# Performance work log

Measured on AMD Instinct MI355X. Metric: run time of the kernel, lower is better.

Reference implementation:

```python
import jax, jax.numpy as jnp
import numpy as np

N, F, H, L, O, E = 20000, 128, 128, 4, 64, 640000
NEG_SLOPE = 0.2  # PyG GATConv default


def setup_inputs() -> dict:
    key = jax.random.key(0)
    ks = jax.random.split(key, 8)
    x = jax.random.normal(ks[0], (N, F), dtype=jnp.float32)
    edge_index = jax.random.randint(ks[1], (2, E), 0, N, dtype=jnp.int64)
    sc = 1.0 / np.sqrt(F)
    Ws = jax.random.normal(ks[2], (L, F, H), dtype=jnp.float32) * sc
    att_src = jax.random.normal(ks[3], (L, H), dtype=jnp.float32) * sc
    att_dst = jax.random.normal(ks[4], (L, H), dtype=jnp.float32) * sc
    biases = jnp.zeros((L, H), dtype=jnp.float32)
    W_out = jax.random.normal(ks[5], (H, O), dtype=jnp.float32) * (1.0 / np.sqrt(H))
    b_out = jnp.zeros((O,), dtype=jnp.float32)
    return {"x": x, "edge_index": edge_index, "Ws": Ws, "att_src": att_src,
            "att_dst": att_dst, "biases": biases, "W_out": W_out, "b_out": b_out}


def _gat_conv(h, src, dst, W, a_s, a_d, b):
    # h: [N, F_in]; single-head GATConv (PyG semantics)
    z = h @ W                                   # [N, H]
    alpha_s = z @ a_s                           # [N]
    alpha_d = z @ a_d                           # [N]
    logits = jax.nn.leaky_relu(alpha_s[src] + alpha_d[dst], negative_slope=NEG_SLOPE)  # [E']
    # segment-softmax over edges grouped by destination node
    m = jax.ops.segment_max(logits, dst, num_segments=N)
    p = jnp.exp(logits - m[dst])
    s = jax.ops.segment_sum(p, dst, num_segments=N)
    alpha = p / (s[dst] + 1e-16)                # [E']
    out = jax.ops.segment_sum(alpha[:, None] * z[src], dst, num_segments=N)  # [N, H]
    return out + b


def reference(x, edge_index, Ws, att_src, att_dst, biases, W_out, b_out):
    # add self-loops once (PyG GATConv default add_self_loops=True)
    loop = jnp.arange(N, dtype=edge_index.dtype)
    src = jnp.concatenate([edge_index[0], loop])
    dst = jnp.concatenate([edge_index[1], loop])
    h = x
    for l in range(L):
        h = _gat_conv(h, src, dst, Ws[l], att_src[l], att_dst[l], biases[l])
        h = jax.nn.relu(h)  # Dropout is identity at eval
    return h @ W_out + b_out  # [N, O]
```

## Files before the change

### kernel.cpp

```cpp
#include <hip/hip_runtime.h>

#define NN 20000
#define FF 128
#define HH 128
#define LL 4
#define OO 64
#define EE 640000
#define NEG 0.2f
#define NB ((NN + 255) / 256)

typedef short bf16x8 __attribute__((ext_vector_type(8)));
typedef float f32x4 __attribute__((ext_vector_type(4)));

__device__ inline ushort f2bf(float f) {
    uint u = __float_as_uint(f);
    return (ushort)((u + 0x7fffu + ((u >> 16) & 1u)) >> 16);
}


__global__ void k_init_counters(int* __restrict__ counters) {
    int i = blockIdx.x * 256 + threadIdx.x;
    if (i < NN) counters[i] = 1;
}

__global__ void k_hist(const int* __restrict__ dst, int* __restrict__ counters) {
    int e = blockIdx.x * 256 + threadIdx.x;
    if (e < EE) atomicAdd(&counters[dst[e]], 1);
}

__global__ void k_partial(const int* __restrict__ counters, int* __restrict__ partials) {
    __shared__ int ws[4];
    int t = threadIdx.x;
    int i = blockIdx.x * 256 + t;
    int c = (i < NN) ? counters[i] : 0;
    #pragma unroll
    for (int off = 32; off; off >>= 1) c += __shfl_xor(c, off);
    if ((t & 63) == 0) ws[t >> 6] = c;
    __syncthreads();
    if (t == 0) partials[blockIdx.x] = ws[0] + ws[1] + ws[2] + ws[3];
}

__global__ void k_scan_small(const int* __restrict__ partials, int* __restrict__ offsets) {
    __shared__ int sp[128];
    int t = threadIdx.x;
    int v = (t < NB) ? partials[t] : 0;
    sp[t] = v;
    __syncthreads();
    for (int off = 1; off < 128; off <<= 1) {
        int u = (t >= off) ? sp[t - off] : 0;
        __syncthreads();
        sp[t] += u;
        __syncthreads();
    }
    if (t < NB) offsets[t] = sp[t] - v;
}

__global__ void k_apply(const int* __restrict__ counters, const int* __restrict__ offsets,
                        int* __restrict__ row_off, int* __restrict__ cursor,
                        int* __restrict__ src_sorted) {
    __shared__ int sc[256];
    int t = threadIdx.x;
    int i = blockIdx.x * 256 + t;
    int c = (i < NN) ? counters[i] : 0;
    sc[t] = c;
    __syncthreads();
    for (int off = 1; off < 256; off <<= 1) {
        int u = (t >= off) ? sc[t - off] : 0;
        __syncthreads();
        sc[t] += u;
        __syncthreads();
    }
    int incl = sc[t];
    int base = offsets[blockIdx.x];
    if (i < NN) {
        int excl = base + incl - c;
        row_off[i] = excl;
        cursor[i] = excl + 1;
        src_sorted[excl] = i;
        if (i == NN - 1) row_off[NN] = base + incl;
    }
}

__global__ void k_scatter(const int* __restrict__ src, const int* __restrict__ dst,
                          int* __restrict__ cursor, int* __restrict__ src_sorted) {
    int e = blockIdx.x * 256 + threadIdx.x;
    if (e < EE) {
        int p = atomicAdd(&cursor[dst[e]], 1);
        src_sorted[p] = src[e];
    }
}


__global__ void k_convw(const float* __restrict__ Ws, const float* __restrict__ Wout,
                        ushort* __restrict__ wh, ushort* __restrict__ wl) {
    int idx = blockIdx.x * 256 + threadIdx.x;
    const int per_l = HH * 128;
    float v;
    if (idx < LL * per_l) {
        int l = idx / per_l, rem = idx % per_l;
        int n = rem >> 7, k = rem & 127;
        v = Ws[(size_t)l * 128 * HH + (size_t)k * HH + n];
    } else {
        int j = idx - LL * per_l;
        if (j >= OO * 128) return;
        int n = j >> 7, k = j & 127;
        v = Wout[(size_t)k * OO + n];
    }
    ushort h = f2bf(v);
    float hf = __uint_as_float((uint)h << 16);
    wh[idx] = h;
    wl[idx] = f2bf(v - hf);
}


__global__ void k_wa(const float* __restrict__ Ws, const float* __restrict__ attS,
                     const float* __restrict__ attD, float* __restrict__ wa) {
    int t = blockIdx.x * 256 + threadIdx.x;
    if (t >= LL * 256) return;
    int l = t >> 8, rem = t & 255, which = rem >> 7, k = rem & 127;
    const float* wrow = Ws + (size_t)l * 128 * HH + (size_t)k * HH;
    const float* av = (which ? attD : attS) + l * HH;
    float s = 0.f;
    #pragma unroll 4
    for (int n = 0; n < HH; n++) s += wrow[n] * av[n];
    wa[l * 256 + which * 128 + k] = s;
}


template <int NCOL, bool BIAS, bool ALPHAS>
__global__ void k_gemm_mfma(const float* __restrict__ A, const ushort* __restrict__ wh,
                            const ushort* __restrict__ wl, const float* __restrict__ bias,
                            float* __restrict__ C, const float* __restrict__ wa,
                            float* __restrict__ as_out, float* __restrict__ ad_out) {
    constexpr int CT = NCOL / 32;
    int bid = blockIdx.x;
    int rt = bid / CT, ct = bid % CT;
    int l = threadIdx.x;
    int row0 = rt * 16, col0 = ct * 32;
    int lr = l & 15, lg = l >> 4;

    const float* arow = A + (size_t)(row0 + lr) * 128;
    f32x4 af0[4], af1[4];
    #pragma unroll
    for (int s = 0; s < 4; s++) {
        af0[s] = *(const f32x4*)(arow + s * 32 + lg * 8);
        af1[s] = *(const f32x4*)(arow + s * 32 + lg * 8 + 4);
    }
    bf16x8 ah[4], al[4];
    #pragma unroll
    for (int s = 0; s < 4; s++) {
        #pragma unroll
        for (int j = 0; j < 8; j++) {
            float v = (j < 4) ? af0[s][j] : af1[s][j - 4];
            ushort h = f2bf(v);
            float hf = __uint_as_float((uint)h << 16);
            ah[s][j] = (short)h;
            al[s][j] = (short)f2bf(v - hf);
        }
    }

    f32x4 acc[2] = {{0.f, 0.f, 0.f, 0.f}, {0.f, 0.f, 0.f, 0.f}};

    #pragma unroll
    for (int s = 0; s < 4; s++) {
        #pragma unroll
        for (int nt = 0; nt < 2; nt++) {
            int woff = (col0 + nt * 16 + lr) * 128 + s * 32 + lg * 8;
            bf16x8 bh = *(const bf16x8*)(wh + woff);
            bf16x8 bl = *(const bf16x8*)(wl + woff);
            acc[nt] = __builtin_amdgcn_mfma_f32_16x16x32_bf16(ah[s], bh, acc[nt], 0, 0, 0);
            acc[nt] = __builtin_amdgcn_mfma_f32_16x16x32_bf16(ah[s], bl, acc[nt], 0, 0, 0);
            acc[nt] = __builtin_amdgcn_mfma_f32_16x16x32_bf16(al[s], bh, acc[nt], 0, 0, 0);
        }
    }

    int orow = lg * 4;
    #pragma unroll
    for (int nt = 0; nt < 2; nt++) {
        #pragma unroll
        for (int r = 0; r < 4; r++) {
            float v = acc[nt][r];
            if (BIAS) v += bias[col0 + nt * 16 + lr];
            C[(size_t)(row0 + orow + r) * NCOL + col0 + nt * 16 + lr] = v;
        }
    }

    if constexpr (ALPHAS) {
        if (ct == 0) {
            float ps = 0.f, pd = 0.f;
            #pragma unroll
            for (int s = 0; s < 4; s++) {
                #pragma unroll
                for (int j = 0; j < 8; j++) {
                    float v = (j < 4) ? af0[s][j] : af1[s][j - 4];
                    int k = s * 32 + lg * 8 + j;
                    ps += v * wa[k];
                    pd += v * wa[128 + k];
                }
            }
            ps += __shfl_xor(ps, 16);  pd += __shfl_xor(pd, 16);
            ps += __shfl_xor(ps, 32);  pd += __shfl_xor(pd, 32);
            if (lg == 0) {
                as_out[row0 + lr] = ps;
                ad_out[row0 + lr] = pd;
            }
        }
    }
}


__global__ void k_aggregate(const float* __restrict__ z, const float* __restrict__ as,
                            const float* __restrict__ ad, const int* __restrict__ row_off,
                            const int* __restrict__ srcs, const float* __restrict__ bias,
                            float* __restrict__ out) {
    int node = blockIdx.x * 4 + (threadIdx.x >> 6);
    int lane = threadIdx.x & 63;
    if (node >= NN) return;
    int beg = row_off[node], end = row_off[node + 1];
    float adn = ad[node];
    float lself = as[node] + adn;
    float mx = (lself >= 0.f) ? lself : NEG * lself;

    int g = lane >> 5, cl = lane & 31;
    const float4* zb = (const float4*)z;
    float4 acc = make_float4(0.f, 0.f, 0.f, 0.f);
    float s = 0.f;

    for (int e = beg + g; e < end; e += 16) {
        int e1 = e + 2, e2 = e + 4, e3 = e + 6, e4 = e + 8, e5 = e + 10, e6 = e + 12, e7 = e + 14;
        int lim = end - 1;
        int i1 = min(e1, lim), i2 = min(e2, lim), i3 = min(e3, lim);
        int i4 = min(e4, lim), i5 = min(e5, lim), i6 = min(e6, lim), i7 = min(e7, lim);
        int s0 = srcs[e], s1 = srcs[i1], s2 = srcs[i2], s3 = srcs[i3];
        int s4 = srcs[i4], s5 = srcs[i5], s6 = srcs[i6], s7 = srcs[i7];
        float l0 = as[s0] + adn, l1 = as[s1] + adn, l2 = as[s2] + adn, l3 = as[s3] + adn;
        float l4 = as[s4] + adn, l5 = as[s5] + adn, l6 = as[s6] + adn, l7 = as[s7] + adn;
        l0 = (l0 >= 0.f) ? l0 : NEG * l0;  l1 = (l1 >= 0.f) ? l1 : NEG * l1;
        l2 = (l2 >= 0.f) ? l2 : NEG * l2;  l3 = (l3 >= 0.f) ? l3 : NEG * l3;
        l4 = (l4 >= 0.f) ? l4 : NEG * l4;  l5 = (l5 >= 0.f) ? l5 : NEG * l5;
        l6 = (l6 >= 0.f) ? l6 : NEG * l6;  l7 = (l7 >= 0.f) ? l7 : NEG * l7;
        float4 z0 = zb[(size_t)s0 * 32 + cl];
        float4 z1 = zb[(size_t)s1 * 32 + cl];
        float4 z2 = zb[(size_t)s2 * 32 + cl];
        float4 z3 = zb[(size_t)s3 * 32 + cl];
        float4 z4 = zb[(size_t)s4 * 32 + cl];
        float4 z5 = zb[(size_t)s5 * 32 + cl];
        float4 z6 = zb[(size_t)s6 * 32 + cl];
        float4 z7 = zb[(size_t)s7 * 32 + cl];
        float p0 = __expf(l0 - mx);
        float p1 = (e1 < end) ? __expf(l1 - mx) : 0.f;
        float p2 = (e2 < end) ? __expf(l2 - mx) : 0.f;
        float p3 = (e3 < end) ? __expf(l3 - mx) : 0.f;
        float p4 = (e4 < end) ? __expf(l4 - mx) : 0.f;
        float p5 = (e5 < end) ? __expf(l5 - mx) : 0.f;
        float p6 = (e6 < end) ? __expf(l6 - mx) : 0.f;
        float p7 = (e7 < end) ? __expf(l7 - mx) : 0.f;
        s += ((p0 + p1) + (p2 + p3)) + ((p4 + p5) + (p6 + p7));
        acc.x += (p0 * z0.x + p1 * z1.x + p2 * z2.x + p3 * z3.x)
               + (p4 * z4.x + p5 * z5.x + p6 * z6.x + p7 * z7.x);
        acc.y += (p0 * z0.y + p1 * z1.y + p2 * z2.y + p3 * z3.y)
               + (p4 * z4.y + p5 * z5.y + p6 * z6.y + p7 * z7.y);
        acc.z += (p0 * z0.z + p1 * z1.z + p2 * z2.z + p3 * z3.z)
               + (p4 * z4.z + p5 * z5.z + p6 * z6.z + p7 * z7.z);
        acc.w += (p0 * z0.w + p1 * z1.w + p2 * z2.w + p3 * z3.w)
               + (p4 * z4.w + p5 * z5.w + p6 * z6.w + p7 * z7.w);
    }

    acc.x += __shfl_xor(acc.x, 32);
    acc.y += __shfl_xor(acc.y, 32);
    acc.z += __shfl_xor(acc.z, 32);
    acc.w += __shfl_xor(acc.w, 32);
    s     += __shfl_xor(s, 32);

    if (g == 0) {
        float inv = 1.f / (s + 1e-16f);
        float4 b = ((const float4*)bias)[cl];
        float4 o;
        o.x = fmaxf(acc.x * inv + b.x, 0.f);
        o.y = fmaxf(acc.y * inv + b.y, 0.f);
        o.z = fmaxf(acc.z * inv + b.z, 0.f);
        o.w = fmaxf(acc.w * inv + b.w, 0.f);
        ((float4*)out)[(size_t)node * 32 + cl] = o;
    }
}


extern "C" void kernel_launch(void* const* d_in, const int* in_sizes, int n_in,
                              void* d_out, int out_size, void* d_ws, size_t ws_size,
                              hipStream_t stream) {
    const float* x      = (const float*)d_in[0];
    const int*   ei     = (const int*)d_in[1];
    const float* Ws     = (const float*)d_in[2];
    const float* attS   = (const float*)d_in[3];
    const float* attD   = (const float*)d_in[4];
    const float* biases = (const float*)d_in[5];
    const float* W_out  = (const float*)d_in[6];
    const float* b_out  = (const float*)d_in[7];
    float* out = (float*)d_out;

    const int* srcp = ei;
    const int* dstp = ei + EE;

    char* w = (char*)d_ws;
    auto take = [&](size_t bytes) {
        char* p = w;
        w += (bytes + 15) & ~(size_t)15;
        return p;
    };
    float*  zbuf       = (float*)take((size_t)NN * HH * 4);
    float*  hbuf       = (float*)take((size_t)NN * HH * 4);
    float*  as_v       = (float*)take((size_t)NN * 4);
    float*  ad_v       = (float*)take((size_t)NN * 4);
    int*    counters   = (int*)take((size_t)NN * 4);
    int*    row_off    = (int*)take((size_t)(NN + 1) * 4);
    int*    cursor     = (int*)take((size_t)NN * 4);
    int*    src_sorted = (int*)take((size_t)(EE + NN) * 4);
    int*    partials   = (int*)take((size_t)NB * 4);
    int*    offsets    = (int*)take((size_t)NB * 4);
    const int WTOT = LL * HH * 128 + OO * 128;
    ushort* whbuf      = (ushort*)take((size_t)WTOT * 2);
    ushort* wlbuf      = (ushort*)take((size_t)WTOT * 2);
    float*  wabuf      = (float*)take((size_t)LL * 256 * 4);

    k_init_counters<<<(NN + 255) / 256, 256, 0, stream>>>(counters);
    k_hist<<<(EE + 255) / 256, 256, 0, stream>>>(dstp, counters);
    k_partial<<<NB, 256, 0, stream>>>(counters, partials);
    k_scan_small<<<1, 128, 0, stream>>>(partials, offsets);
    k_apply<<<NB, 256, 0, stream>>>(counters, offsets, row_off, cursor, src_sorted);
    k_scatter<<<(EE + 255) / 256, 256, 0, stream>>>(srcp, dstp, cursor, src_sorted);
    k_convw<<<(WTOT + 255) / 256, 256, 0, stream>>>(Ws, W_out, whbuf, wlbuf);
    k_wa<<<(LL * 256 + 255) / 256, 256, 0, stream>>>(Ws, attS, attD, wabuf);

    const int node_blocks = (NN + 3) / 4;

    for (int l = 0; l < LL; l++) {
        const float* hin = (l == 0) ? x : hbuf;
        k_gemm_mfma<HH, false, true><<<(NN / 16) * (HH / 32), 64, 0, stream>>>(
            hin, whbuf + (size_t)l * HH * 128, wlbuf + (size_t)l * HH * 128,
            nullptr, zbuf, wabuf + l * 256, as_v, ad_v);
        k_aggregate<<<node_blocks, 256, 0, stream>>>(zbuf, as_v, ad_v, row_off, src_sorted,
                                                     biases + l * HH, hbuf);
    }

    k_gemm_mfma<OO, true, false><<<(NN / 16) * (OO / 32), 64, 0, stream>>>(
        hbuf, whbuf + (size_t)LL * HH * 128, wlbuf + (size_t)LL * HH * 128,
        b_out, out, nullptr, nullptr, nullptr);
}
```

Baseline: 329.9 us.

## Fuse aggregation with next layer's GEMM via shared-memory tile

```diff
diff --git a/kernel.cpp b/kernel.cpp
--- a/kernel.cpp
+++ b/kernel.cpp
@@ -8,6 +8,7 @@
 #define EE 640000
 #define NEG 0.2f
 #define NB ((NN + 255) / 256)
+#define NTILES (NN / 16)
 
 typedef short bf16x8 __attribute__((ext_vector_type(8)));
 typedef float f32x4 __attribute__((ext_vector_type(4)));
@@ -127,24 +128,95 @@
 }
 
 
+__device__ inline void do_agg(const float* __restrict__ z, const float* __restrict__ as,
+                              const float* __restrict__ ad, const int* __restrict__ row_off,
+                              const int* __restrict__ srcs, const float* __restrict__ bias,
+                              float (*h)[132], int node0, int wid, int l64) {
+    int g = l64 >> 5, cl = l64 & 31;
+    const float4* zb = (const float4*)z;
+    #pragma unroll 1
+    for (int i = 0; i < 4; i++) {
+        int node = node0 + wid * 4 + i;
+        int beg = row_off[node], end = row_off[node + 1];
+        float adn = ad[node];
+        float lself = as[node] + adn;
+        float mx = (lself >= 0.f) ? lself : NEG * lself;
+
+        float4 acc = make_float4(0.f, 0.f, 0.f, 0.f);
+        float s = 0.f;
+        for (int e = beg + g; e < end; e += 16) {
+            int e1 = e + 2, e2 = e + 4, e3 = e + 6, e4 = e + 8, e5 = e + 10, e6 = e + 12, e7 = e + 14;
+            int lim = end - 1;
+            int i1 = min(e1, lim), i2 = min(e2, lim), i3 = min(e3, lim);
+            int i4 = min(e4, lim), i5 = min(e5, lim), i6 = min(e6, lim), i7 = min(e7, lim);
+            int s0 = srcs[e], s1 = srcs[i1], s2 = srcs[i2], s3 = srcs[i3];
+            int s4 = srcs[i4], s5 = srcs[i5], s6 = srcs[i6], s7 = srcs[i7];
+            float l0 = as[s0] + adn, l1 = as[s1] + adn, l2 = as[s2] + adn, l3 = as[s3] + adn;
+            float l4 = as[s4] + adn, l5 = as[s5] + adn, l6 = as[s6] + adn, l7 = as[s7] + adn;
+            l0 = (l0 >= 0.f) ? l0 : NEG * l0;  l1 = (l1 >= 0.f) ? l1 : NEG * l1;
+            l2 = (l2 >= 0.f) ? l2 : NEG * l2;  l3 = (l3 >= 0.f) ? l3 : NEG * l3;
+            l4 = (l4 >= 0.f) ? l4 : NEG * l4;  l5 = (l5 >= 0.f) ? l5 : NEG * l5;
+            l6 = (l6 >= 0.f) ? l6 : NEG * l6;  l7 = (l7 >= 0.f) ? l7 : NEG * l7;
+            float4 z0 = zb[(size_t)s0 * 32 + cl];
+            float4 z1 = zb[(size_t)s1 * 32 + cl];
+            float4 z2 = zb[(size_t)s2 * 32 + cl];
+            float4 z3 = zb[(size_t)s3 * 32 + cl];
+            float4 z4 = zb[(size_t)s4 * 32 + cl];
+            float4 z5 = zb[(size_t)s5 * 32 + cl];
+            float4 z6 = zb[(size_t)s6 * 32 + cl];
+            float4 z7 = zb[(size_t)s7 * 32 + cl];
+            float p0 = __expf(l0 - mx);
+            float p1 = (e1 < end) ? __expf(l1 - mx) : 0.f;
+            float p2 = (e2 < end) ? __expf(l2 - mx) : 0.f;
+            float p3 = (e3 < end) ? __expf(l3 - mx) : 0.f;
+            float p4 = (e4 < end) ? __expf(l4 - mx) : 0.f;
+            float p5 = (e5 < end) ? __expf(l5 - mx) : 0.f;
+            float p6 = (e6 < end) ? __expf(l6 - mx) : 0.f;
+            float p7 = (e7 < end) ? __expf(l7 - mx) : 0.f;
+            s += ((p0 + p1) + (p2 + p3)) + ((p4 + p5) + (p6 + p7));
+            acc.x += (p0 * z0.x + p1 * z1.x + p2 * z2.x + p3 * z3.x)
+                   + (p4 * z4.x + p5 * z5.x + p6 * z6.x + p7 * z7.x);
+            acc.y += (p0 * z0.y + p1 * z1.y + p2 * z2.y + p3 * z3.y)
+                   + (p4 * z4.y + p5 * z5.y + p6 * z6.y + p7 * z7.y);
+            acc.z += (p0 * z0.z + p1 * z1.z + p2 * z2.z + p3 * z3.z)
+                   + (p4 * z4.z + p5 * z5.z + p6 * z6.z + p7 * z7.z);
+            acc.w += (p0 * z0.w + p1 * z1.w + p2 * z2.w + p3 * z3.w)
+                   + (p4 * z4.w + p5 * z5.w + p6 * z6.w + p7 * z7.w);
+        }
+        acc.x += __shfl_xor(acc.x, 32);
+        acc.y += __shfl_xor(acc.y, 32);
+        acc.z += __shfl_xor(acc.z, 32);
+        acc.w += __shfl_xor(acc.w, 32);
+        s     += __shfl_xor(s, 32);
+        if (g == 0) {
+            float inv = 1.f / (s + 1e-16f);
+            float4 b = ((const float4*)bias)[cl];
+            int lrow = wid * 4 + i;
+            h[lrow][cl * 4 + 0] = fmaxf(acc.x * inv + b.x, 0.f);
+            h[lrow][cl * 4 + 1] = fmaxf(acc.y * inv + b.y, 0.f);
+            h[lrow][cl * 4 + 2] = fmaxf(acc.z * inv + b.z, 0.f);
+            h[lrow][cl * 4 + 3] = fmaxf(acc.w * inv + b.w, 0.f);
+        }
+    }
+}
+
 template <int NCOL, bool BIAS, bool ALPHAS>
-__global__ void k_gemm_mfma(const float* __restrict__ A, const ushort* __restrict__ wh,
-                            const ushort* __restrict__ wl, const float* __restrict__ bias,
-                            float* __restrict__ C, const float* __restrict__ wa,
-                            float* __restrict__ as_out, float* __restrict__ ad_out) {
+__device__ inline void do_gemm(const float (*h)[132], const ushort* __restrict__ wh,
+                               const ushort* __restrict__ wl, const float* __restrict__ bias,
+                               float* __restrict__ C, const float* __restrict__ wa,
+                               float* __restrict__ as_o, float* __restrict__ ad_o,
+                               int row0, int wid, int l64) {
     constexpr int CT = NCOL / 32;
-    int bid = blockIdx.x;
-    int rt = bid / CT, ct = bid % CT;
-    int l = threadIdx.x;
-    int row0 = rt * 16, col0 = ct * 32;
-    int lr = l & 15, lg = l >> 4;
-
-    const float* arow = A + (size_t)(row0 + lr) * 128;
+    if (CT < 4 && wid >= CT) return;
+    int ct = wid;
+    int lr = l64 & 15, lg = l64 >> 4;
+    int col0 = ct * 32;
+
     f32x4 af0[4], af1[4];
     #pragma unroll
     for (int s = 0; s < 4; s++) {
-        af0[s] = *(const f32x4*)(arow + s * 32 + lg * 8);
-        af1[s] = *(const f32x4*)(arow + s * 32 + lg * 8 + 4);
+        af0[s] = *(const f32x4*)&h[lr][s * 32 + lg * 8];
+        af1[s] = *(const f32x4*)&h[lr][s * 32 + lg * 8 + 4];
     }
     bf16x8 ah[4], al[4];
     #pragma unroll
@@ -152,15 +224,14 @@
         #pragma unroll
         for (int j = 0; j < 8; j++) {
             float v = (j < 4) ? af0[s][j] : af1[s][j - 4];
-            ushort h = f2bf(v);
-            float hf = __uint_as_float((uint)h << 16);
-            ah[s][j] = (short)h;
+            ushort hb = f2bf(v);
+            float hf = __uint_as_float((uint)hb << 16);
+            ah[s][j] = (short)hb;
             al[s][j] = (short)f2bf(v - hf);
         }
     }
 
     f32x4 acc[2] = {{0.f, 0.f, 0.f, 0.f}, {0.f, 0.f, 0.f, 0.f}};
-
     #pragma unroll
     for (int s = 0; s < 4; s++) {
         #pragma unroll
@@ -201,87 +272,43 @@
             ps += __shfl_xor(ps, 16);  pd += __shfl_xor(pd, 16);
             ps += __shfl_xor(ps, 32);  pd += __shfl_xor(pd, 32);
             if (lg == 0) {
-                as_out[row0 + lr] = ps;
-                ad_out[row0 + lr] = pd;
+                as_o[row0 + lr] = ps;
+                ad_o[row0 + lr] = pd;
             }
         }
     }
 }
 
 
-__global__ void k_aggregate(const float* __restrict__ z, const float* __restrict__ as,
-                            const float* __restrict__ ad, const int* __restrict__ row_off,
-                            const int* __restrict__ srcs, const float* __restrict__ bias,
-                            float* __restrict__ out) {
-    int node = blockIdx.x * 4 + (threadIdx.x >> 6);
-    int lane = threadIdx.x & 63;
-    if (node >= NN) return;
-    int beg = row_off[node], end = row_off[node + 1];
-    float adn = ad[node];
-    float lself = as[node] + adn;
-    float mx = (lself >= 0.f) ? lself : NEG * lself;
-
-    int g = lane >> 5, cl = lane & 31;
-    const float4* zb = (const float4*)z;
-    float4 acc = make_float4(0.f, 0.f, 0.f, 0.f);
-    float s = 0.f;
-
-    for (int e = beg + g; e < end; e += 16) {
-        int e1 = e + 2, e2 = e + 4, e3 = e + 6, e4 = e + 8, e5 = e + 10, e6 = e + 12, e7 = e + 14;
-        int lim = end - 1;
-        int i1 = min(e1, lim), i2 = min(e2, lim), i3 = min(e3, lim);
-        int i4 = min(e4, lim), i5 = min(e5, lim), i6 = min(e6, lim), i7 = min(e7, lim);
-        int s0 = srcs[e], s1 = srcs[i1], s2 = srcs[i2], s3 = srcs[i3];
-        int s4 = srcs[i4], s5 = srcs[i5], s6 = srcs[i6], s7 = srcs[i7];
-        float l0 = as[s0] + adn, l1 = as[s1] + adn, l2 = as[s2] + adn, l3 = as[s3] + adn;
-        float l4 = as[s4] + adn, l5 = as[s5] + adn, l6 = as[s6] + adn, l7 = as[s7] + adn;
-        l0 = (l0 >= 0.f) ? l0 : NEG * l0;  l1 = (l1 >= 0.f) ? l1 : NEG * l1;
-        l2 = (l2 >= 0.f) ? l2 : NEG * l2;  l3 = (l3 >= 0.f) ? l3 : NEG * l3;
-        l4 = (l4 >= 0.f) ? l4 : NEG * l4;  l5 = (l5 >= 0.f) ? l5 : NEG * l5;
-        l6 = (l6 >= 0.f) ? l6 : NEG * l6;  l7 = (l7 >= 0.f) ? l7 : NEG * l7;
-        float4 z0 = zb[(size_t)s0 * 32 + cl];
-        float4 z1 = zb[(size_t)s1 * 32 + cl];
-        float4 z2 = zb[(size_t)s2 * 32 + cl];
-        float4 z3 = zb[(size_t)s3 * 32 + cl];
-        float4 z4 = zb[(size_t)s4 * 32 + cl];
-        float4 z5 = zb[(size_t)s5 * 32 + cl];
-        float4 z6 = zb[(size_t)s6 * 32 + cl];
-        float4 z7 = zb[(size_t)s7 * 32 + cl];
-        float p0 = __expf(l0 - mx);
-        float p1 = (e1 < end) ? __expf(l1 - mx) : 0.f;
-        float p2 = (e2 < end) ? __expf(l2 - mx) : 0.f;
-        float p3 = (e3 < end) ? __expf(l3 - mx) : 0.f;
-        float p4 = (e4 < end) ? __expf(l4 - mx) : 0.f;
-        float p5 = (e5 < end) ? __expf(l5 - mx) : 0.f;
-        float p6 = (e6 < end) ? __expf(l6 - mx) : 0.f;
-        float p7 = (e7 < end) ? __expf(l7 - mx) : 0.f;
-        s += ((p0 + p1) + (p2 + p3)) + ((p4 + p5) + (p6 + p7));
-        acc.x += (p0 * z0.x + p1 * z1.x + p2 * z2.x + p3 * z3.x)
-               + (p4 * z4.x + p5 * z5.x + p6 * z6.x + p7 * z7.x);
-        acc.y += (p0 * z0.y + p1 * z1.y + p2 * z2.y + p3 * z3.y)
-               + (p4 * z4.y + p5 * z5.y + p6 * z6.y + p7 * z7.y);
-        acc.z += (p0 * z0.z + p1 * z1.z + p2 * z2.z + p3 * z3.z)
-               + (p4 * z4.z + p5 * z5.z + p6 * z6.z + p7 * z7.z);
-        acc.w += (p0 * z0.w + p1 * z1.w + p2 * z2.w + p3 * z3.w)
-               + (p4 * z4.w + p5 * z5.w + p6 * z6.w + p7 * z7.w);
-    }
-
-    acc.x += __shfl_xor(acc.x, 32);
-    acc.y += __shfl_xor(acc.y, 32);
-    acc.z += __shfl_xor(acc.z, 32);
-    acc.w += __shfl_xor(acc.w, 32);
-    s     += __shfl_xor(s, 32);
-
-    if (g == 0) {
-        float inv = 1.f / (s + 1e-16f);
-        float4 b = ((const float4*)bias)[cl];
-        float4 o;
-        o.x = fmaxf(acc.x * inv + b.x, 0.f);
-        o.y = fmaxf(acc.y * inv + b.y, 0.f);
-        o.z = fmaxf(acc.z * inv + b.z, 0.f);
-        o.w = fmaxf(acc.w * inv + b.w, 0.f);
-        ((float4*)out)[(size_t)node * 32 + cl] = o;
-    }
+__global__ __launch_bounds__(256)
+void k_layer0(const float* __restrict__ x, const ushort* __restrict__ wh,
+              const ushort* __restrict__ wl, const float* __restrict__ wa,
+              float* __restrict__ z, float* __restrict__ as_o, float* __restrict__ ad_o) {
+    __shared__ float h[16][132];
+    int t = threadIdx.x, wid = t >> 6, l64 = t & 63;
+    int row0 = blockIdx.x * 16;
+    for (int i = t; i < 16 * 32; i += 256) {
+        int r = i >> 5, c4 = (i & 31) << 2;
+        *(float4*)&h[r][c4] = *(const float4*)&x[(size_t)(row0 + r) * 128 + c4];
+    }
+    __syncthreads();
+    do_gemm<HH, false, true>(h, wh, wl, nullptr, z, wa, as_o, ad_o, row0, wid, l64);
+}
+
+template <int NCOL, bool BIAS, bool ALPHAS>
+__global__ __launch_bounds__(256)
+void k_layer(const float* __restrict__ zin, const float* __restrict__ asi,
+             const float* __restrict__ adi, const int* __restrict__ row_off,
+             const int* __restrict__ srcs, const float* __restrict__ abias,
+             const ushort* __restrict__ wh, const ushort* __restrict__ wl,
+             const float* __restrict__ cbias, const float* __restrict__ wa,
+             float* __restrict__ zout, float* __restrict__ as_o, float* __restrict__ ad_o) {
+    __shared__ float h[16][132];
+    int t = threadIdx.x, wid = t >> 6, l64 = t & 63;
+    int row0 = blockIdx.x * 16;
+    do_agg(zin, asi, adi, row_off, srcs, abias, h, row0, wid, l64);
+    __syncthreads();
+    do_gemm<NCOL, BIAS, ALPHAS>(h, wh, wl, cbias, zout, wa, as_o, ad_o, row0, wid, l64);
 }
 
 
@@ -307,10 +334,12 @@
         w += (bytes + 15) & ~(size_t)15;
         return p;
     };
-    float*  zbuf       = (float*)take((size_t)NN * HH * 4);
-    float*  hbuf       = (float*)take((size_t)NN * HH * 4);
-    float*  as_v       = (float*)take((size_t)NN * 4);
-    float*  ad_v       = (float*)take((size_t)NN * 4);
+    float*  za         = (float*)take((size_t)NN * HH * 4);
+    float*  zbv        = (float*)take((size_t)NN * HH * 4);
+    float*  asa        = (float*)take((size_t)NN * 4);
+    float*  ada        = (float*)take((size_t)NN * 4);
+    float*  asb        = (float*)take((size_t)NN * 4);
+    float*  adb        = (float*)take((size_t)NN * 4);
     int*    counters   = (int*)take((size_t)NN * 4);
     int*    row_off    = (int*)take((size_t)(NN + 1) * 4);
     int*    cursor     = (int*)take((size_t)NN * 4);
@@ -331,18 +360,23 @@
     k_convw<<<(WTOT + 255) / 256, 256, 0, stream>>>(Ws, W_out, whbuf, wlbuf);
     k_wa<<<(LL * 256 + 255) / 256, 256, 0, stream>>>(Ws, attS, attD, wabuf);
 
-    const int node_blocks = (NN + 3) / 4;
-
-    for (int l = 0; l < LL; l++) {
-        const float* hin = (l == 0) ? x : hbuf;
-        k_gemm_mfma<HH, false, true><<<(NN / 16) * (HH / 32), 64, 0, stream>>>(
-            hin, whbuf + (size_t)l * HH * 128, wlbuf + (size_t)l * HH * 128,
-            nullptr, zbuf, wabuf + l * 256, as_v, ad_v);
-        k_aggregate<<<node_blocks, 256, 0, stream>>>(zbuf, as_v, ad_v, row_off, src_sorted,
-                                                     biases + l * HH, hbuf);
-    }
-
-    k_gemm_mfma<OO, true, false><<<(NN / 16) * (OO / 32), 64, 0, stream>>>(
-        hbuf, whbuf + (size_t)LL * HH * 128, wlbuf + (size_t)LL * HH * 128,
-        b_out, out, nullptr, nullptr, nullptr);
-}
+    k_layer0<<<NTILES, 256, 0, stream>>>(x, whbuf, wlbuf, wabuf, za, asa, ada);
+
+    k_layer<HH, false, true><<<NTILES, 256, 0, stream>>>(
+        za, asa, ada, row_off, src_sorted, biases + 0 * HH,
+        whbuf + (size_t)1 * HH * 128, wlbuf + (size_t)1 * HH * 128,
+        nullptr, wabuf + 1 * 256, zbv, asb, adb);
+    k_layer<HH, false, true><<<NTILES, 256, 0, stream>>>(
+        zbv, asb, adb, row_off, src_sorted, biases + 1 * HH,
+        whbuf + (size_t)2 * HH * 128, wlbuf + (size_t)2 * HH * 128,
+        nullptr, wabuf + 2 * 256, za, asa, ada);
+    k_layer<HH, false, true><<<NTILES, 256, 0, stream>>>(
+        za, asa, ada, row_off, src_sorted, biases + 2 * HH,
+        whbuf + (size_t)3 * HH * 128, wlbuf + (size_t)3 * HH * 128,
+        nullptr, wabuf + 3 * 256, zbv, asb, adb);
+
+    k_layer<OO, true, false><<<NTILES, 256, 0, stream>>>(
+        zbv, asb, adb, row_off, src_sorted, biases + 3 * HH,
+        whbuf + (size_t)LL * HH * 128, wlbuf + (size_t)LL * HH * 128,
+        b_out, nullptr, out, nullptr, nullptr);
+}
```

Measured after the change: 377.2 us. 14.3% more time.

## Precompute edge softmax weights per layer and restructure GEMM to stage rows in LDS

Applied to the files above, without the earlier changes.

```diff
diff --git a/kernel.cpp b/kernel.cpp
--- a/kernel.cpp
+++ b/kernel.cpp
@@ -6,8 +6,10 @@
 #define LL 4
 #define OO 64
 #define EE 640000
+#define ET (EE + NN)
 #define NEG 0.2f
 #define NB ((NN + 255) / 256)
+#define NTILES (NN / 16)
 
 typedef short bf16x8 __attribute__((ext_vector_type(8)));
 typedef float f32x4 __attribute__((ext_vector_type(4)));
@@ -57,7 +59,7 @@
 
 __global__ void k_apply(const int* __restrict__ counters, const int* __restrict__ offsets,
                         int* __restrict__ row_off, int* __restrict__ cursor,
-                        int* __restrict__ src_sorted) {
+                        int* __restrict__ src_sorted, int* __restrict__ dst_sorted) {
     __shared__ int sc[256];
     int t = threadIdx.x;
     int i = blockIdx.x * 256 + t;
@@ -77,16 +79,20 @@
         row_off[i] = excl;
         cursor[i] = excl + 1;
         src_sorted[excl] = i;
+        dst_sorted[excl] = i;
         if (i == NN - 1) row_off[NN] = base + incl;
     }
 }
 
 __global__ void k_scatter(const int* __restrict__ src, const int* __restrict__ dst,
-                          int* __restrict__ cursor, int* __restrict__ src_sorted) {
+                          int* __restrict__ cursor, int* __restrict__ src_sorted,
+                          int* __restrict__ dst_sorted) {
     int e = blockIdx.x * 256 + threadIdx.x;
     if (e < EE) {
-        int p = atomicAdd(&cursor[dst[e]], 1);
-        src_sorted[p] = src[e];
+        int d = dst[e];
+        int pidx = atomicAdd(&cursor[d], 1);
+        src_sorted[pidx] = src[e];
+        dst_sorted[pidx] = d;
     }
 }
 
@@ -127,24 +133,109 @@
 }
 
 
+__global__ void k_ew(const float* __restrict__ asv, const float* __restrict__ adv,
+                     const int* __restrict__ srcs, const int* __restrict__ dsts,
+                     float* __restrict__ p) {
+    int e = blockIdx.x * 256 + threadIdx.x;
+    if (e >= ET) return;
+    int s = srcs[e], d = dsts[e];
+    float ad_ = adv[d];
+    float ls = asv[s] + ad_;  ls = (ls >= 0.f) ? ls : NEG * ls;
+    float ld = asv[d] + ad_;  ld = (ld >= 0.f) ? ld : NEG * ld;
+    p[e] = __expf(ls - ld);
+}
+
+
+__global__ __launch_bounds__(256)
+void k_agg(const float* __restrict__ z, const float* __restrict__ p,
+           const int* __restrict__ row_off, const int* __restrict__ srcs,
+           const float* __restrict__ bias, float* __restrict__ h) {
+    int node = blockIdx.x * 4 + (threadIdx.x >> 6);
+    int l64 = threadIdx.x & 63;
+    if (node >= NN) return;
+    int g = l64 >> 5, cl = l64 & 31;
+    int beg = row_off[node], end = row_off[node + 1], lim = end - 1;
+    const float4* zb = (const float4*)z;
+
+    float4 acc = make_float4(0.f, 0.f, 0.f, 0.f);
+    float s = 0.f;
+    for (int e = beg + g * 8; e < end; e += 16) {
+        int i1 = min(e + 1, lim), i2 = min(e + 2, lim), i3 = min(e + 3, lim);
+        int i4 = min(e + 4, lim), i5 = min(e + 5, lim), i6 = min(e + 6, lim), i7 = min(e + 7, lim);
+        int s0 = srcs[e],  s1 = srcs[i1], s2 = srcs[i2], s3 = srcs[i3];
+        int s4 = srcs[i4], s5 = srcs[i5], s6 = srcs[i6], s7 = srcs[i7];
+        float p0 = p[e];
+        float p1 = (e + 1 < end) ? p[e + 1] : 0.f;
+        float p2 = (e + 2 < end) ? p[e + 2] : 0.f;
+        float p3 = (e + 3 < end) ? p[e + 3] : 0.f;
+        float p4 = (e + 4 < end) ? p[e + 4] : 0.f;
+        float p5 = (e + 5 < end) ? p[e + 5] : 0.f;
+        float p6 = (e + 6 < end) ? p[e + 6] : 0.f;
+        float p7 = (e + 7 < end) ? p[e + 7] : 0.f;
+        float4 z0 = zb[(size_t)s0 * 32 + cl];
+        float4 z1 = zb[(size_t)s1 * 32 + cl];
+        float4 z2 = zb[(size_t)s2 * 32 + cl];
+        float4 z3 = zb[(size_t)s3 * 32 + cl];
+        float4 z4 = zb[(size_t)s4 * 32 + cl];
+        float4 z5 = zb[(size_t)s5 * 32 + cl];
+        float4 z6 = zb[(size_t)s6 * 32 + cl];
+        float4 z7 = zb[(size_t)s7 * 32 + cl];
+        s += ((p0 + p1) + (p2 + p3)) + ((p4 + p5) + (p6 + p7));
+        acc.x += (p0 * z0.x + p1 * z1.x + p2 * z2.x + p3 * z3.x)
+               + (p4 * z4.x + p5 * z5.x + p6 * z6.x + p7 * z7.x);
+        acc.y += (p0 * z0.y + p1 * z1.y + p2 * z2.y + p3 * z3.y)
+               + (p4 * z4.y + p5 * z5.y + p6 * z6.y + p7 * z7.y);
+        acc.z += (p0 * z0.z + p1 * z1.z + p2 * z2.z + p3 * z3.z)
+               + (p4 * z4.z + p5 * z5.z + p6 * z6.z + p7 * z7.z);
+        acc.w += (p0 * z0.w + p1 * z1.w + p2 * z2.w + p3 * z3.w)
+               + (p4 * z4.w + p5 * z5.w + p6 * z6.w + p7 * z7.w);
+    }
+
+    acc.x += __shfl_xor(acc.x, 32);
+    acc.y += __shfl_xor(acc.y, 32);
+    acc.z += __shfl_xor(acc.z, 32);
+    acc.w += __shfl_xor(acc.w, 32);
+    s     += __shfl_xor(s, 32);
+
+    if (g == 0) {
+        float inv = 1.f / (s + 1e-16f);
+        float4 b = ((const float4*)bias)[cl];
+        float4 o;
+        o.x = fmaxf(acc.x * inv + b.x, 0.f);
+        o.y = fmaxf(acc.y * inv + b.y, 0.f);
+        o.z = fmaxf(acc.z * inv + b.z, 0.f);
+        o.w = fmaxf(acc.w * inv + b.w, 0.f);
+        ((float4*)h)[(size_t)node * 32 + cl] = o;
+    }
+}
+
+
 template <int NCOL, bool BIAS, bool ALPHAS>
-__global__ void k_gemm_mfma(const float* __restrict__ A, const ushort* __restrict__ wh,
-                            const ushort* __restrict__ wl, const float* __restrict__ bias,
-                            float* __restrict__ C, const float* __restrict__ wa,
-                            float* __restrict__ as_out, float* __restrict__ ad_out) {
+__global__ __launch_bounds__(256)
+void k_gemm2(const float* __restrict__ A, const ushort* __restrict__ wh,
+             const ushort* __restrict__ wl, const float* __restrict__ bias,
+             float* __restrict__ C, const float* __restrict__ wa,
+             float* __restrict__ as_o, float* __restrict__ ad_o) {
+    __shared__ float h[16][132];
+    int t = threadIdx.x;
+    int row0 = blockIdx.x * 16;
+    for (int i = t; i < 512; i += 256) {
+        int r = i >> 5, c4 = (i & 31) << 2;
+        *(float4*)&h[r][c4] = *(const float4*)&A[(size_t)(row0 + r) * 128 + c4];
+    }
+    __syncthreads();
+
+    int wid = t >> 6, l64 = t & 63;
     constexpr int CT = NCOL / 32;
-    int bid = blockIdx.x;
-    int rt = bid / CT, ct = bid % CT;
-    int l = threadIdx.x;
-    int row0 = rt * 16, col0 = ct * 32;
-    int lr = l & 15, lg = l >> 4;
-
-    const float* arow = A + (size_t)(row0 + lr) * 128;
+    if (wid >= CT) return;
+    int lr = l64 & 15, lg = l64 >> 4;
+    int col0 = wid * 32;
+
     f32x4 af0[4], af1[4];
     #pragma unroll
     for (int s = 0; s < 4; s++) {
-        af0[s] = *(const f32x4*)(arow + s * 32 + lg * 8);
-        af1[s] = *(const f32x4*)(arow + s * 32 + lg * 8 + 4);
+        af0[s] = *(const f32x4*)&h[lr][s * 32 + lg * 8];
+        af1[s] = *(const f32x4*)&h[lr][s * 32 + lg * 8 + 4];
     }
     bf16x8 ah[4], al[4];
     #pragma unroll
@@ -152,15 +243,14 @@
         #pragma unroll
         for (int j = 0; j < 8; j++) {
             float v = (j < 4) ? af0[s][j] : af1[s][j - 4];
-            ushort h = f2bf(v);
-            float hf = __uint_as_float((uint)h << 16);
-            ah[s][j] = (short)h;
+            ushort hb = f2bf(v);
+            float hf = __uint_as_float((uint)hb << 16);
+            ah[s][j] = (short)hb;
             al[s][j] = (short)f2bf(v - hf);
         }
     }
 
     f32x4 acc[2] = {{0.f, 0.f, 0.f, 0.f}, {0.f, 0.f, 0.f, 0.f}};
-
     #pragma unroll
     for (int s = 0; s < 4; s++) {
         #pragma unroll
@@ -177,16 +267,17 @@
     int orow = lg * 4;
     #pragma unroll
     for (int nt = 0; nt < 2; nt++) {
+        int c = col0 + nt * 16 + lr;
         #pragma unroll
         for (int r = 0; r < 4; r++) {
             float v = acc[nt][r];
-            if (BIAS) v += bias[col0 + nt * 16 + lr];
-            C[(size_t)(row0 + orow + r) * NCOL + col0 + nt * 16 + lr] = v;
+            if (BIAS) v += bias[c];
+            C[(size_t)(row0 + orow + r) * NCOL + c] = v;
         }
     }
 
     if constexpr (ALPHAS) {
-        if (ct == 0) {
+        if (wid == 0) {
             float ps = 0.f, pd = 0.f;
             #pragma unroll
             for (int s = 0; s < 4; s++) {
@@ -201,86 +292,10 @@
             ps += __shfl_xor(ps, 16);  pd += __shfl_xor(pd, 16);
             ps += __shfl_xor(ps, 32);  pd += __shfl_xor(pd, 32);
             if (lg == 0) {
-                as_out[row0 + lr] = ps;
-                ad_out[row0 + lr] = pd;
+                as_o[row0 + lr] = ps;
+                ad_o[row0 + lr] = pd;
             }
         }
-    }
-}
-
-
-__global__ void k_aggregate(const float* __restrict__ z, const float* __restrict__ as,
-                            const float* __restrict__ ad, const int* __restrict__ row_off,
-                            const int* __restrict__ srcs, const float* __restrict__ bias,
-                            float* __restrict__ out) {
-    int node = blockIdx.x * 4 + (threadIdx.x >> 6);
-    int lane = threadIdx.x & 63;
-    if (node >= NN) return;
-    int beg = row_off[node], end = row_off[node + 1];
-    float adn = ad[node];
-    float lself = as[node] + adn;
-    float mx = (lself >= 0.f) ? lself : NEG * lself;
-
-    int g = lane >> 5, cl = lane & 31;
-    const float4* zb = (const float4*)z;
-    float4 acc = make_float4(0.f, 0.f, 0.f, 0.f);
-    float s = 0.f;
-
-    for (int e = beg + g; e < end; e += 16) {
-        int e1 = e + 2, e2 = e + 4, e3 = e + 6, e4 = e + 8, e5 = e + 10, e6 = e + 12, e7 = e + 14;
-        int lim = end - 1;
-        int i1 = min(e1, lim), i2 = min(e2, lim), i3 = min(e3, lim);
-        int i4 = min(e4, lim), i5 = min(e5, lim), i6 = min(e6, lim), i7 = min(e7, lim);
-        int s0 = srcs[e], s1 = srcs[i1], s2 = srcs[i2], s3 = srcs[i3];
-        int s4 = srcs[i4], s5 = srcs[i5], s6 = srcs[i6], s7 = srcs[i7];
-        float l0 = as[s0] + adn, l1 = as[s1] + adn, l2 = as[s2] + adn, l3 = as[s3] + adn;
-        float l4 = as[s4] + adn, l5 = as[s5] + adn, l6 = as[s6] + adn, l7 = as[s7] + adn;
-        l0 = (l0 >= 0.f) ? l0 : NEG * l0;  l1 = (l1 >= 0.f) ? l1 : NEG * l1;
-        l2 = (l2 >= 0.f) ? l2 : NEG * l2;  l3 = (l3 >= 0.f) ? l3 : NEG * l3;
-        l4 = (l4 >= 0.f) ? l4 : NEG * l4;  l5 = (l5 >= 0.f) ? l5 : NEG * l5;
-        l6 = (l6 >= 0.f) ? l6 : NEG * l6;  l7 = (l7 >= 0.f) ? l7 : NEG * l7;
-        float4 z0 = zb[(size_t)s0 * 32 + cl];
-        float4 z1 = zb[(size_t)s1 * 32 + cl];
-        float4 z2 = zb[(size_t)s2 * 32 + cl];
-        float4 z3 = zb[(size_t)s3 * 32 + cl];
-        float4 z4 = zb[(size_t)s4 * 32 + cl];
-        float4 z5 = zb[(size_t)s5 * 32 + cl];
-        float4 z6 = zb[(size_t)s6 * 32 + cl];
-        float4 z7 = zb[(size_t)s7 * 32 + cl];
-        float p0 = __expf(l0 - mx);
-        float p1 = (e1 < end) ? __expf(l1 - mx) : 0.f;
-        float p2 = (e2 < end) ? __expf(l2 - mx) : 0.f;
-        float p3 = (e3 < end) ? __expf(l3 - mx) : 0.f;
-        float p4 = (e4 < end) ? __expf(l4 - mx) : 0.f;
-        float p5 = (e5 < end) ? __expf(l5 - mx) : 0.f;
-        float p6 = (e6 < end) ? __expf(l6 - mx) : 0.f;
-        float p7 = (e7 < end) ? __expf(l7 - mx) : 0.f;
-        s += ((p0 + p1) + (p2 + p3)) + ((p4 + p5) + (p6 + p7));
-        acc.x += (p0 * z0.x + p1 * z1.x + p2 * z2.x + p3 * z3.x)
-               + (p4 * z4.x + p5 * z5.x + p6 * z6.x + p7 * z7.x);
-        acc.y += (p0 * z0.y + p1 * z1.y + p2 * z2.y + p3 * z3.y)
-               + (p4 * z4.y + p5 * z5.y + p6 * z6.y + p7 * z7.y);
-        acc.z += (p0 * z0.z + p1 * z1.z + p2 * z2.z + p3 * z3.z)
-               + (p4 * z4.z + p5 * z5.z + p6 * z6.z + p7 * z7.z);
-        acc.w += (p0 * z0.w + p1 * z1.w + p2 * z2.w + p3 * z3.w)
-               + (p4 * z4.w + p5 * z5.w + p6 * z6.w + p7 * z7.w);
-    }
-
-    acc.x += __shfl_xor(acc.x, 32);
-    acc.y += __shfl_xor(acc.y, 32);
-    acc.z += __shfl_xor(acc.z, 32);
-    acc.w += __shfl_xor(acc.w, 32);
-    s     += __shfl_xor(s, 32);
-
-    if (g == 0) {
-        float inv = 1.f / (s + 1e-16f);
-        float4 b = ((const float4*)bias)[cl];
-        float4 o;
-        o.x = fmaxf(acc.x * inv + b.x, 0.f);
-        o.y = fmaxf(acc.y * inv + b.y, 0.f);
-        o.z = fmaxf(acc.z * inv + b.z, 0.f);
-        o.w = fmaxf(acc.w * inv + b.w, 0.f);
-        ((float4*)out)[(size_t)node * 32 + cl] = o;
     }
 }
 
@@ -307,14 +322,19 @@
         w += (bytes + 15) & ~(size_t)15;
         return p;
     };
-    float*  zbuf       = (float*)take((size_t)NN * HH * 4);
+    float*  za         = (float*)take((size_t)NN * HH * 4);
+    float*  zbv        = (float*)take((size_t)NN * HH * 4);
     float*  hbuf       = (float*)take((size_t)NN * HH * 4);
-    float*  as_v       = (float*)take((size_t)NN * 4);
-    float*  ad_v       = (float*)take((size_t)NN * 4);
+    float*  asa        = (float*)take((size_t)NN * 4);
+    float*  ada        = (float*)take((size_t)NN * 4);
+    float*  asb        = (float*)take((size_t)NN * 4);
+    float*  adb        = (float*)take((size_t)NN * 4);
     int*    counters   = (int*)take((size_t)NN * 4);
     int*    row_off    = (int*)take((size_t)(NN + 1) * 4);
     int*    cursor     = (int*)take((size_t)NN * 4);
-    int*    src_sorted = (int*)take((size_t)(EE + NN) * 4);
+    int*    src_sorted = (int*)take((size_t)ET * 4);
+    int*    dst_sorted = (int*)take((size_t)ET * 4);
+    float*  pbuf       = (float*)take((size_t)ET * 4);
     int*    partials   = (int*)take((size_t)NB * 4);
     int*    offsets    = (int*)take((size_t)NB * 4);
     const int WTOT = LL * HH * 128 + OO * 128;
@@ -326,23 +346,38 @@
     k_hist<<<(EE + 255) / 256, 256, 0, stream>>>(dstp, counters);
     k_partial<<<NB, 256, 0, stream>>>(counters, partials);
     k_scan_small<<<1, 128, 0, stream>>>(partials, offsets);
-    k_apply<<<NB, 256, 0, stream>>>(counters, offsets, row_off, cursor, src_sorted);
-    k_scatter<<<(EE + 255) / 256, 256, 0, stream>>>(srcp, dstp, cursor, src_sorted);
+    k_apply<<<NB, 256, 0, stream>>>(counters, offsets, row_off, cursor,
+                                    src_sorted, dst_sorted);
+    k_scatter<<<(EE + 255) / 256, 256, 0, stream>>>(srcp, dstp, cursor,
+                                                    src_sorted, dst_sorted);
     k_convw<<<(WTOT + 255) / 256, 256, 0, stream>>>(Ws, W_out, whbuf, wlbuf);
     k_wa<<<(LL * 256 + 255) / 256, 256, 0, stream>>>(Ws, attS, attD, wabuf);
 
-    const int node_blocks = (NN + 3) / 4;
-
-    for (int l = 0; l < LL; l++) {
-        const float* hin = (l == 0) ? x : hbuf;
-        k_gemm_mfma<HH, false, true><<<(NN / 16) * (HH / 32), 64, 0, stream>>>(
-            hin, whbuf + (size_t)l * HH * 128, wlbuf + (size_t)l * HH * 128,
-            nullptr, zbuf, wabuf + l * 256, as_v, ad_v);
-        k_aggregate<<<node_blocks, 256, 0, stream>>>(zbuf, as_v, ad_v, row_off, src_sorted,
-                                                     biases + l * HH, hbuf);
-    }
-
-    k_gemm_mfma<OO, true, false><<<(NN / 16) * (OO / 32), 64, 0, stream>>>(
+    const int agg_blocks = (NN + 3) / 4;
+    const int ew_blocks  = (ET + 255) / 256;
+
+    k_gemm2<HH, false, true><<<NTILES, 256, 0, stream>>>(
+        x, whbuf, wlbuf, nullptr, za, wabuf, asa, ada);
+
+    const float* zi[3]  = {za, zbv, za};
+    float*       zo[3]  = {zbv, za, zbv};
+    const float* asi[3] = {asa, asb, asa};
+    const float* adi[3] = {ada, adb, ada};
+    float*       aso[3] = {asb, asa, asb};
+    float*       ado[3] = {adb, ada, adb};
+    for (int l = 0; l < 3; l++) {
+        k_ew<<<ew_blocks, 256, 0, stream>>>(asi[l], adi[l], src_sorted, dst_sorted, pbuf);
+        k_agg<<<agg_blocks, 256, 0, stream>>>(zi[l], pbuf, row_off, src_sorted,
+                                              biases + l * HH, hbuf);
+        k_gemm2<HH, false, true><<<NTILES, 256, 0, stream>>>(
+            hbuf, whbuf + (size_t)(l + 1) * HH * 128, wlbuf + (size_t)(l + 1) * HH * 128,
+            nullptr, zo[l], wabuf + (l + 1) * 256, aso[l], ado[l]);
+    }
+
+    k_ew<<<ew_blocks, 256, 0, stream>>>(asb, adb, src_sorted, dst_sorted, pbuf);
+    k_agg<<<agg_blocks, 256, 0, stream>>>(zbv, pbuf, row_off, src_sorted,
+                                          biases + 3 * HH, hbuf);
+    k_gemm2<OO, true, false><<<NTILES, 256, 0, stream>>>(
         hbuf, whbuf + (size_t)LL * HH * 128, wlbuf + (size_t)LL * HH * 128,
         b_out, out, nullptr, nullptr, nullptr);
 }
```

Result: faster. 317.9 us (-3.7%).
